# Kernel optimization log

Hardware: AMD Instinct MI355X
Metric: run time of the kernel (lower is better)

The kernel has to match this reference:

```python
import jax, jax.numpy as jnp
import numpy as np

NUM_GRAPHS = 2500  # number of graphs in the batch (Set2Set segments)
DIM = 64


def _forward(x, edge_attr, lin0_w, lin0_b, mlp1_w, mlp1_b, mlp2_w, mlp2_b,
             root_w, conv_b, gru_w_ih, gru_w_hh, gru_b_ih, gru_b_hh,
             lstm_w_ih, lstm_w_hh, lstm_b_ih, lstm_b_hh, lin1_w, lin1_b,
             edge_index, batch):
    D = DIM
    N = x.shape[0]
    src, dst = edge_index[0], edge_index[1]

    out = jax.nn.relu(x @ lin0_w.T + lin0_b)        # [N, D]
    h = out                                          # GRU hidden state

    # Edge-conditioned weights: nn(edge_attr).view(E, in, out). Identical each
    # layer in the original (same edge_attr), so compute once.
    ew = jax.nn.relu(edge_attr @ mlp1_w.T + mlp1_b)  # [E, 128]
    ew = (ew @ mlp2_w.T + mlp2_b).reshape(-1, D, D)  # [E, D, D]

    deg = jax.ops.segment_sum(jnp.ones_like(dst, jnp.float32), dst, N)
    deg = jnp.clip(deg, 1.0)                         # mean aggregation denom

    for _ in range(3):
        # NNConv: gather source feats, per-edge matmul, scatter-mean to targets
        msg = jnp.einsum('ei,eio->eo', out[src], ew)          # [E, D]
        agg = jax.ops.segment_sum(msg, dst, N) / deg[:, None]  # [N, D]
        m = jax.nn.relu(agg + out @ root_w.T + conv_b)
        # GRU step (torch gate order: r, z, n)
        gi = m @ gru_w_ih.T + gru_b_ih
        gh = h @ gru_w_hh.T + gru_b_hh
        ir, iz, inn = jnp.split(gi, 3, axis=-1)
        hr, hz, hn = jnp.split(gh, 3, axis=-1)
        r = jax.nn.sigmoid(ir + hr)
        z = jax.nn.sigmoid(iz + hz)
        n = jnp.tanh(inn + r * hn)
        h = (1.0 - z) * n + z * h
        out = h

    # Set2Set pooling, 3 processing steps (LSTM: in 2D -> hidden D)
    B = NUM_GRAPHS
    q_star = jnp.zeros((B, 2 * D), x.dtype)
    hl = jnp.zeros((B, D), x.dtype)
    cl = jnp.zeros((B, D), x.dtype)
    for _ in range(3):
        gates = q_star @ lstm_w_ih.T + lstm_b_ih + hl @ lstm_w_hh.T + lstm_b_hh
        i_, f_, g_, o_ = jnp.split(gates, 4, axis=-1)  # torch order i,f,g,o
        cl = jax.nn.sigmoid(f_) * cl + jax.nn.sigmoid(i_) * jnp.tanh(g_)
        hl = jax.nn.sigmoid(o_) * jnp.tanh(cl)
        q = hl                                          # [B, D]
        e = jnp.sum(out * q[batch], axis=-1)            # [N]
        emax = jax.ops.segment_max(e, batch, B)
        a = jnp.exp(e - emax[batch])
        a = a / jax.ops.segment_sum(a, batch, B)[batch]
        r_ = jax.ops.segment_sum(a[:, None] * out, batch, B)  # [B, D]
        q_star = jnp.concatenate([q, r_], axis=-1)      # [B, 2D]

    return jax.nn.relu(q_star @ lin1_w.T + lin1_b)      # [B, D]


def setup_inputs() -> dict:
    key = jax.random.key(0)
    ks = jax.random.split(key, 16)
    N, E, F_, D, EA = 50000, 100000, 11, DIM, 5

    def g(k, shape, scale=0.05):
        return jax.random.normal(k, shape, dtype=jnp.float32) * scale

    return dict(
        x=jax.random.normal(ks[0], (N, F_), dtype=jnp.float32),
        edge_attr=jax.random.uniform(ks[1], (E, EA), dtype=jnp.float32),
        lin0_w=g(ks[2], (D, F_)), lin0_b=jnp.zeros((D,), jnp.float32),
        mlp1_w=g(ks[3], (128, EA)), mlp1_b=jnp.zeros((128,), jnp.float32),
        mlp2_w=g(ks[4], (D * D, 128), 0.01), mlp2_b=jnp.zeros((D * D,), jnp.float32),
        root_w=g(ks[5], (D, D)), conv_b=jnp.zeros((D,), jnp.float32),
        gru_w_ih=g(ks[6], (3 * D, D)), gru_w_hh=g(ks[7], (3 * D, D)),
        gru_b_ih=jnp.zeros((3 * D,), jnp.float32), gru_b_hh=jnp.zeros((3 * D,), jnp.float32),
        lstm_w_ih=g(ks[8], (4 * D, 2 * D)), lstm_w_hh=g(ks[9], (4 * D, D)),
        lstm_b_ih=jnp.zeros((4 * D,), jnp.float32), lstm_b_hh=jnp.zeros((4 * D,), jnp.float32),
        lin1_w=g(ks[10], (D, 2 * D)), lin1_b=jnp.zeros((D,), jnp.float32),
        edge_index=jax.random.randint(ks[11], (2, E), 0, N),
        batch=jnp.sort(jax.random.randint(ks[12], (N,), 0, NUM_GRAPHS)),
    )


def reference(x, edge_attr, lin0_w, lin0_b, mlp1_w, mlp1_b, mlp2_w, mlp2_b,
              root_w, conv_b, gru_w_ih, gru_w_hh, gru_b_ih, gru_b_hh,
              lstm_w_ih, lstm_w_hh, lstm_b_ih, lstm_b_hh, lin1_w, lin1_b,
              edge_index, batch):
    return _forward(x, edge_attr, lin0_w, lin0_b, mlp1_w, mlp1_b, mlp2_w, mlp2_b,
                    root_w, conv_b, gru_w_ih, gru_w_hh, gru_b_ih, gru_b_hh,
                    lstm_w_ih, lstm_w_hh, lstm_b_ih, lstm_b_hh, lin1_w, lin1_b,
                    edge_index, batch)
```

## Files before the change

### kernel.cpp

```cpp
#include <hip/hip_runtime.h>
#include <hip/hip_bf16.h>
#include <stdint.h>


#define N_NODES 50000
#define N_EDGES 100000
#define NGRAPH  2500
#define FIN     11
#define EATT    5

typedef __attribute__((ext_vector_type(8))) short short8;
typedef __attribute__((ext_vector_type(4))) float f32x4;

__device__ __forceinline__ short8 zero8(){ short8 z = {0,0,0,0,0,0,0,0}; return z; }

__device__ __forceinline__ unsigned short f2bf(float x){
  unsigned u = __float_as_uint(x);
  u += 0x7FFFu + ((u >> 16) & 1u);
  return (unsigned short)(u >> 16);
}
__device__ __forceinline__ float sigm(float x){ return 1.0f/(1.0f+__expf(-x)); }

#define FB_CVT   2160
#define FB_LIN0  12500
#define FB_MLP1  50000
#define FB_DEG   391
__global__ void k_front(const float* __restrict__ x, const float* __restrict__ l0w,
        const float* __restrict__ l0b, float* __restrict__ out, unsigned short* __restrict__ outb,
        const float* __restrict__ ea, const float* __restrict__ m1w, const float* __restrict__ m1b,
        unsigned short* __restrict__ hidb, const int* __restrict__ dst, float* __restrict__ deg,
        const float* __restrict__ mlp2w, const float* __restrict__ rootw,
        const float* __restrict__ wih, const float* __restrict__ whh,
        unsigned short* __restrict__ w2b, unsigned short* __restrict__ rootb,
        unsigned short* __restrict__ wihb, unsigned short* __restrict__ whhb){
  int bb = blockIdx.x;
  if (bb < FB_CVT){
    int i = bb*256 + threadIdx.x;
    if (i < 524288) w2b[i] = f2bf(mlp2w[i]);
    else if (i < 528384) rootb[i-524288] = f2bf(rootw[i-524288]);
    else if (i < 540672) wihb[i-528384] = f2bf(wih[i-528384]);
    else                 whhb[i-540672] = f2bf(whh[i-540672]);
  } else if (bb < FB_CVT + FB_LIN0){
    int t = (bb-FB_CVT)*256 + threadIdx.x;
    int n = t >> 6, o = t & 63;
    float s = l0b[o];
    #pragma unroll
    for (int f = 0; f < FIN; ++f) s += x[n*FIN+f]*l0w[o*FIN+f];
    s = fmaxf(s, 0.f);
    out[(size_t)n*64+o] = s; outb[(size_t)n*64+o] = f2bf(s);
  } else if (bb < FB_CVT + FB_LIN0 + FB_MLP1){
    int t = (bb-FB_CVT-FB_LIN0)*256 + threadIdx.x;
    int e = t >> 7, j = t & 127;
    float s = m1b[j];
    #pragma unroll
    for (int a = 0; a < EATT; ++a) s += ea[e*EATT+a]*m1w[j*EATT+a];
    hidb[(size_t)e*128+j] = f2bf(fmaxf(s,0.f));
  } else {
    int e = (bb-FB_CVT-FB_LIN0-FB_MLP1)*256 + threadIdx.x;
    if (e < N_EDGES) atomicAdd(&deg[dst[e]], 1.0f);
  }
}

__global__ __launch_bounds__(256) void k_msgf(const unsigned short* __restrict__ hidb,
        const unsigned short* __restrict__ w2b, const float* __restrict__ b2,
        const float* __restrict__ out, const int* __restrict__ src,
        const int* __restrict__ dst, float* __restrict__ agg){
  __shared__ unsigned short w2t[2][64*128];
  __shared__ float os[64*65];
  __shared__ int sidx[128];
  int mt = blockIdx.x;
  int tid = threadIdx.x;
  int wave = tid>>6, l = tid&63, lm = l&15, g = l>>4;
  if (tid < 64){
    int e = mt*64 + tid;
    sidx[tid]    = (e < N_EDGES) ? src[e] : -1;
    sidx[64+tid] = (e < N_EDGES) ? dst[e] : -1;
  }
  __syncthreads();
  {
    int el = tid>>2, i0 = (tid&3)*16;
    int sn = sidx[el];
    #pragma unroll
    for (int j = 0; j < 16; j += 4){
      float4 v;
      if (sn >= 0) v = *(const float4*)(out + (size_t)sn*64 + i0 + j);
      else { v.x = v.y = v.z = v.w = 0.f; }
      os[el*65+i0+j]   = v.x; os[el*65+i0+j+1] = v.y;
      os[el*65+i0+j+2] = v.z; os[el*65+i0+j+3] = v.w;
    }
  }
  short8 afr[4];
  {
    int e = mt*64 + wave*16 + lm;
    bool ok = (e < N_EDGES);
    #pragma unroll
    for (int kk = 0; kk < 4; ++kk)
      afr[kk] = ok ? *(const short8*)(hidb + (size_t)e*128 + kk*32 + 8*g) : zero8();
  }
  int srow = tid>>2, sq = tid&3, swz = srow & 7;
  {
    const uint4* gp = (const uint4*)(w2b + (size_t)srow*128 + sq*32);
    uint4 r0 = gp[0], r1 = gp[1], r2 = gp[2], r3 = gp[3];
    unsigned short* lb = &w2t[0][srow*128];
    int c0 = sq*4;
    *(uint4*)(lb + ((((c0+0)^swz))<<3)) = r0;
    *(uint4*)(lb + ((((c0+1)^swz))<<3)) = r1;
    *(uint4*)(lb + ((((c0+2)^swz))<<3)) = r2;
    *(uint4*)(lb + ((((c0+3)^swz))<<3)) = r3;
  }
  __syncthreads();
  float msgacc[4][4];
  #pragma unroll
  for (int t=0;t<4;++t){
    #pragma unroll
    for (int r=0;r<4;++r) msgacc[t][r] = 0.f;
  }
  int swzl = lm & 7;
  for (int i = 0; i < 64; ++i){
    uint4 r0, r1, r2, r3;
    if (i < 63){
      const uint4* gp = (const uint4*)(w2b + (size_t)((i+1)*64 + srow)*128 + sq*32);
      r0 = gp[0]; r1 = gp[1]; r2 = gp[2]; r3 = gp[3];
    }
    const unsigned short* wt = w2t[i&1];
    f32x4 acc[4];
    #pragma unroll
    for (int t=0;t<4;++t){ f32x4 z = {0.f,0.f,0.f,0.f}; acc[t] = z; }
    #pragma unroll
    for (int t = 0; t < 4; ++t){
      #pragma unroll
      for (int kk = 0; kk < 4; ++kk){
        short8 bfr = *(const short8*)(wt + (t*16+lm)*128 + ((((kk<<2)+g)^swzl)<<3));
        acc[t] = __builtin_amdgcn_mfma_f32_16x16x32_bf16(bfr, afr[kk], acc[t], 0,0,0);
      }
    }
    float ov = os[(wave*16+lm)*65 + i];
    #pragma unroll
    for (int t = 0; t < 4; ++t){
      float4 bv = *(const float4*)(b2 + i*64 + t*16 + 4*g);
      msgacc[t][0] += (acc[t][0]+bv.x)*ov;
      msgacc[t][1] += (acc[t][1]+bv.y)*ov;
      msgacc[t][2] += (acc[t][2]+bv.z)*ov;
      msgacc[t][3] += (acc[t][3]+bv.w)*ov;
    }
    if (i < 63){
      unsigned short* lb = &w2t[(i+1)&1][srow*128];
      int c0 = sq*4;
      *(uint4*)(lb + ((((c0+0)^swz))<<3)) = r0;
      *(uint4*)(lb + ((((c0+1)^swz))<<3)) = r1;
      *(uint4*)(lb + ((((c0+2)^swz))<<3)) = r2;
      *(uint4*)(lb + ((((c0+3)^swz))<<3)) = r3;
    }
    __syncthreads();
  }
  #pragma unroll
  for (int t = 0; t < 4; ++t){
    #pragma unroll
    for (int r = 0; r < 4; ++r)
      os[(wave*16+lm)*65 + t*16 + 4*g + r] = msgacc[t][r];
  }
  __syncthreads();
  {
    int el = tid>>2, o0 = (tid&3)*16;
    int dn = sidx[64+el];
    if (dn >= 0){
      float* ap = agg + (size_t)dn*64 + o0;
      #pragma unroll
      for (int j = 0; j < 16; ++j) atomicAdd(ap + j, os[el*65+o0+j]);
    }
  }
}

__global__ __launch_bounds__(256) void k_update(float* __restrict__ out, unsigned short* __restrict__ outb,
        float* __restrict__ agg, const float* __restrict__ deg,
        const unsigned short* __restrict__ rootb, const float* __restrict__ convb,
        const unsigned short* __restrict__ wihb, const unsigned short* __restrict__ whhb,
        const float* __restrict__ bih, const float* __restrict__ bhh){
  __shared__ unsigned short ms_[4][1024];
  int wave = threadIdx.x >> 6;
  int l = threadIdx.x & 63;
  int lm = l & 15, g = l >> 4;
  int m0 = blockIdx.x*64 + wave*16;
  short8 ah[2];
  {
    int r = m0 + lm; bool ok = r < N_NODES;
    #pragma unroll
    for (int kk = 0; kk < 2; ++kk)
      ah[kk] = ok ? *(const short8*)(outb + (size_t)r*64 + kk*32 + 8*g) : zero8();
  }
  float dinv[4];
  #pragma unroll
  for (int i = 0; i < 4; ++i){
    int r = m0 + 4*g + i;
    dinv[i] = 1.0f / fmaxf((r < N_NODES) ? deg[r] : 1.f, 1.0f);
  }
  #pragma unroll
  for (int nt = 0; nt < 4; ++nt){
    f32x4 acc = {0.f,0.f,0.f,0.f};
    #pragma unroll
    for (int kk = 0; kk < 2; ++kk){
      short8 b = *(const short8*)(rootb + (size_t)(nt*16+lm)*64 + kk*32 + 8*g);
      acc = __builtin_amdgcn_mfma_f32_16x16x32_bf16(ah[kk], b, acc, 0,0,0);
    }
    int c = nt*16 + lm;
    #pragma unroll
    for (int i = 0; i < 4; ++i){
      int lr = 4*g + i, r = m0 + lr;
      float v = 0.f;
      if (r < N_NODES){
        size_t ix = (size_t)r*64 + c;
        v = fmaxf(acc[i] + agg[ix]*dinv[i] + convb[c], 0.f);
        agg[ix] = 0.f;
      }
      ms_[wave][(lr*64 + c) ^ ((lr&7)<<3)] = f2bf(v);
    }
  }
  __syncthreads();
  short8 am[2];
  #pragma unroll
  for (int kk = 0; kk < 2; ++kk)
    am[kk] = *(const short8*)(&ms_[wave][(lm*64 + kk*32 + 8*g) ^ ((lm&7)<<3)]);
  f32x4 accg[12], acch[12];
  #pragma unroll
  for (int nt = 0; nt < 12; ++nt){ f32x4 z = {0.f,0.f,0.f,0.f}; accg[nt]=z; acch[nt]=z; }
  #pragma unroll
  for (int nt = 0; nt < 12; ++nt){
    #pragma unroll
    for (int kk = 0; kk < 2; ++kk){
      short8 bg = *(const short8*)(wihb + (size_t)(nt*16+lm)*64 + kk*32 + 8*g);
      accg[nt] = __builtin_amdgcn_mfma_f32_16x16x32_bf16(am[kk], bg, accg[nt], 0,0,0);
      short8 bh = *(const short8*)(whhb + (size_t)(nt*16+lm)*64 + kk*32 + 8*g);
      acch[nt] = __builtin_amdgcn_mfma_f32_16x16x32_bf16(ah[kk], bh, acch[nt], 0,0,0);
    }
  }
  #pragma unroll
  for (int nt = 0; nt < 4; ++nt){
    int c = nt*16 + lm;
    #pragma unroll
    for (int i = 0; i < 4; ++i){
      int r = m0 + 4*g + i;
      if (r < N_NODES){
        float ir = accg[nt][i]   + bih[c],     hr = acch[nt][i]   + bhh[c];
        float iz = accg[nt+4][i] + bih[64+c],  hz = acch[nt+4][i] + bhh[64+c];
        float in_= accg[nt+8][i] + bih[128+c], hn = acch[nt+8][i] + bhh[128+c];
        float rr = sigm(ir+hr), zz = sigm(iz+hz);
        float nn = tanhf(in_ + rr*hn);
        float hp = out[(size_t)r*64+c];
        float hv = (1.f-zz)*nn + zz*hp;
        out[(size_t)r*64+c] = hv;
        outb[(size_t)r*64+c] = f2bf(hv);
      }
    }
  }
}

__global__ __launch_bounds__(64) void k_s2s(const float* __restrict__ out,
        const int* __restrict__ batch,
        const float* __restrict__ wih, const float* __restrict__ whh,
        const float* __restrict__ bih, const float* __restrict__ bhh,
        const float* __restrict__ w1, const float* __restrict__ b1,
        float* __restrict__ outp){
  int b = blockIdx.x, o = threadIdx.x;
  int s, e2;
  { int lo = 0, hi = N_NODES;
    while (lo < hi){ int m = (lo+hi)>>1; if (batch[m] < b) lo = m+1; else hi = m; }
    s = lo; hi = N_NODES;
    while (lo < hi){ int m = (lo+hi)>>1; if (batch[m] < b+1) lo = m+1; else hi = m; }
    e2 = lo;
  }
  int cnt = e2 - s;
  __shared__ float sq[128];
  __shared__ float sh[64];
  __shared__ float se[512];
  __shared__ float sinv[1];
  float hl = 0.f, cl = 0.f;
  sq[o] = 0.f; sq[64+o] = 0.f; sh[o] = 0.f;
  __syncthreads();
  for (int step = 0; step < 3; ++step){
    float gi = bih[o]      + bhh[o];
    float gf = bih[64+o]   + bhh[64+o];
    float gg = bih[128+o]  + bhh[128+o];
    float go = bih[192+o]  + bhh[192+o];
    #pragma unroll 4
    for (int k = 0; k < 128; k += 4){
      float4 q4 = *(const float4*)(sq+k);
      float4 a4 = *(const float4*)(wih + (size_t)o*128 + k);
      float4 b4 = *(const float4*)(wih + (size_t)(64+o)*128 + k);
      float4 c4 = *(const float4*)(wih + (size_t)(128+o)*128 + k);
      float4 d4 = *(const float4*)(wih + (size_t)(192+o)*128 + k);
      gi += q4.x*a4.x + q4.y*a4.y + q4.z*a4.z + q4.w*a4.w;
      gf += q4.x*b4.x + q4.y*b4.y + q4.z*b4.z + q4.w*b4.w;
      gg += q4.x*c4.x + q4.y*c4.y + q4.z*c4.z + q4.w*c4.w;
      go += q4.x*d4.x + q4.y*d4.y + q4.z*d4.z + q4.w*d4.w;
    }
    #pragma unroll 4
    for (int k = 0; k < 64; k += 4){
      float4 h4 = *(const float4*)(sh+k);
      float4 a4 = *(const float4*)(whh + (size_t)o*64 + k);
      float4 b4 = *(const float4*)(whh + (size_t)(64+o)*64 + k);
      float4 c4 = *(const float4*)(whh + (size_t)(128+o)*64 + k);
      float4 d4 = *(const float4*)(whh + (size_t)(192+o)*64 + k);
      gi += h4.x*a4.x + h4.y*a4.y + h4.z*a4.z + h4.w*a4.w;
      gf += h4.x*b4.x + h4.y*b4.y + h4.z*b4.z + h4.w*b4.w;
      gg += h4.x*c4.x + h4.y*c4.y + h4.z*c4.z + h4.w*c4.w;
      go += h4.x*d4.x + h4.y*d4.y + h4.z*d4.z + h4.w*d4.w;
    }
    cl = sigm(gf)*cl + sigm(gi)*tanhf(gg);
    hl = sigm(go)*tanhf(cl);
    __syncthreads();
    sh[o] = hl; sq[o] = hl;
    __syncthreads();
    for (int j = o; j < cnt; j += 64){
      const float* op = out + (size_t)(s+j)*64;
      float d = 0.f;
      #pragma unroll 4
      for (int k = 0; k < 64; k += 4){
        float4 v  = *(const float4*)(op+k);
        float4 q4 = *(const float4*)(sq+k);
        d += v.x*q4.x + v.y*q4.y + v.z*q4.z + v.w*q4.w;
      }
      if (j < 512) se[j] = d;
    }
    __syncthreads();
    if (o == 0){
      float mx = -INFINITY;
      int c2 = cnt < 512 ? cnt : 512;
      for (int j = 0; j < c2; ++j) mx = fmaxf(mx, se[j]);
      float sm = 0.f;
      for (int j = 0; j < c2; ++j){ float a = __expf(se[j]-mx); se[j] = a; sm += a; }
      sinv[0] = (c2 > 0) ? 1.0f/sm : 0.f;
    }
    __syncthreads();
    float rv = 0.f;
    { int c2 = cnt < 512 ? cnt : 512;
      for (int j = 0; j < c2; ++j) rv += se[j]*out[(size_t)(s+j)*64 + o]; }
    rv *= sinv[0];
    __syncthreads();
    sq[64+o] = rv;
    __syncthreads();
  }
  float sacc = b1[o];
  #pragma unroll 4
  for (int k = 0; k < 128; k += 4){
    float4 q4 = *(const float4*)(sq+k);
    float4 w4 = *(const float4*)(w1 + (size_t)o*128 + k);
    sacc += q4.x*w4.x + q4.y*w4.y + q4.z*w4.z + q4.w*w4.w;
  }
  outp[(size_t)b*64 + o] = fmaxf(sacc, 0.f);
}

extern "C" void kernel_launch(void* const* d_in, const int* in_sizes, int n_in,
                              void* d_out, int out_size, void* d_ws, size_t ws_size,
                              hipStream_t stream){
  (void)in_sizes; (void)n_in; (void)out_size; (void)ws_size;
  const float* x      = (const float*)d_in[0];
  const float* eattr  = (const float*)d_in[1];
  const float* lin0w  = (const float*)d_in[2];
  const float* lin0b  = (const float*)d_in[3];
  const float* mlp1w  = (const float*)d_in[4];
  const float* mlp1b  = (const float*)d_in[5];
  const float* mlp2w  = (const float*)d_in[6];
  const float* mlp2b_ = (const float*)d_in[7];
  const float* rootw  = (const float*)d_in[8];
  const float* convb  = (const float*)d_in[9];
  const float* gwih   = (const float*)d_in[10];
  const float* gwhh   = (const float*)d_in[11];
  const float* gbih   = (const float*)d_in[12];
  const float* gbhh   = (const float*)d_in[13];
  const float* lwih   = (const float*)d_in[14];
  const float* lwhh   = (const float*)d_in[15];
  const float* lbih   = (const float*)d_in[16];
  const float* lbhh   = (const float*)d_in[17];
  const float* lin1w  = (const float*)d_in[18];
  const float* lin1b  = (const float*)d_in[19];
  const int*   eidx   = (const int*)d_in[20];
  const int*   batch  = (const int*)d_in[21];
  const int* srcp = eidx;
  const int* dstp = eidx + N_EDGES;

  char* ws = (char*)d_ws;
  size_t off = 0;
  auto take = [&](size_t bytes)->char*{
    char* p = ws + off; off = (off + bytes + 255) & ~(size_t)255; return p;
  };
  float* out           = (float*)take((size_t)N_NODES*64*4);
  unsigned short* outb = (unsigned short*)take((size_t)N_NODES*64*2);
  unsigned short* hidb = (unsigned short*)take((size_t)N_EDGES*128*2);
  float* agg           = (float*)take((size_t)N_NODES*64*4);
  float* deg           = (float*)take((size_t)N_NODES*4);
  unsigned short* w2b   = (unsigned short*)take((size_t)524288*2);
  unsigned short* rootb = (unsigned short*)take(4096*2);
  unsigned short* wihb  = (unsigned short*)take(12288*2);
  unsigned short* whhb  = (unsigned short*)take(12288*2);

  hipMemsetAsync(deg, 0, (size_t)N_NODES*4, stream);
  hipMemsetAsync(agg, 0, (size_t)N_NODES*64*4, stream);
  k_front<<<FB_CVT+FB_LIN0+FB_MLP1+FB_DEG,256,0,stream>>>(
      x, lin0w, lin0b, out, outb, eattr, mlp1w, mlp1b, hidb, dstp, deg,
      mlp2w, rootw, gwih, gwhh, w2b, rootb, wihb, whhb);
  for (int layer = 0; layer < 3; ++layer){
    k_msgf<<<(N_EDGES+63)/64,256,0,stream>>>(hidb, w2b, mlp2b_, out, srcp, dstp, agg);
    k_update<<<(N_NODES+63)/64,256,0,stream>>>(out, outb, agg, deg, rootb, convb,
                                               wihb, whhb, gbih, gbhh);
  }
  k_s2s<<<NGRAPH,64,0,stream>>>(out, batch, lwih, lwhh, lbih, lbhh, lin1w, lin1b,
                                (float*)d_out);
}
```

Baseline: 1.837 ms.

## Load mlp2 weight fragments directly from global per wave instead of LDS double-buffer

The edge-message kernel no longer stages the 64x128 mlp2 weight slice into double-buffered shared memory with a per-iteration block barrier. Each wave now owns 16 output columns and reads its weight fragments straight from global memory (mostly cache-resident), while holding A fragments for all 64 edges in registers. This removes the 64 per-iteration __syncthreads and the LDS write traffic. In exchange it raises register pressure (16 short8 A fragments) and relies on cache hits for repeated weight reads across blocks.

```diff
diff --git a/kernel.cpp b/kernel.cpp
--- a/kernel.cpp
+++ b/kernel.cpp
@@ -65,7 +65,6 @@
         const unsigned short* __restrict__ w2b, const float* __restrict__ b2,
         const float* __restrict__ out, const int* __restrict__ src,
         const int* __restrict__ dst, float* __restrict__ agg){
-  __shared__ unsigned short w2t[2][64*128];
   __shared__ float os[64*65];
   __shared__ int sidx[128];
   int mt = blockIdx.x;
@@ -89,75 +88,50 @@
       os[el*65+i0+j+2] = v.z; os[el*65+i0+j+3] = v.w;
     }
   }
-  short8 afr[4];
-  {
-    int e = mt*64 + wave*16 + lm;
+  short8 afr[4][4];
+  #pragma unroll
+  for (int ms = 0; ms < 4; ++ms){
+    int e = mt*64 + ms*16 + lm;
     bool ok = (e < N_EDGES);
     #pragma unroll
     for (int kk = 0; kk < 4; ++kk)
-      afr[kk] = ok ? *(const short8*)(hidb + (size_t)e*128 + kk*32 + 8*g) : zero8();
-  }
-  int srow = tid>>2, sq = tid&3, swz = srow & 7;
-  {
-    const uint4* gp = (const uint4*)(w2b + (size_t)srow*128 + sq*32);
-    uint4 r0 = gp[0], r1 = gp[1], r2 = gp[2], r3 = gp[3];
-    unsigned short* lb = &w2t[0][srow*128];
-    int c0 = sq*4;
-    *(uint4*)(lb + ((((c0+0)^swz))<<3)) = r0;
-    *(uint4*)(lb + ((((c0+1)^swz))<<3)) = r1;
-    *(uint4*)(lb + ((((c0+2)^swz))<<3)) = r2;
-    *(uint4*)(lb + ((((c0+3)^swz))<<3)) = r3;
-  }
-  __syncthreads();
-  float msgacc[4][4];
-  #pragma unroll
-  for (int t=0;t<4;++t){
-    #pragma unroll
-    for (int r=0;r<4;++r) msgacc[t][r] = 0.f;
-  }
-  int swzl = lm & 7;
+      afr[ms][kk] = ok ? *(const short8*)(hidb + (size_t)e*128 + kk*32 + 8*g) : zero8();
+  }
+  __syncthreads();
+  f32x4 msgacc[4];
+  #pragma unroll
+  for (int ms=0;ms<4;++ms){ f32x4 z = {0.f,0.f,0.f,0.f}; msgacc[ms] = z; }
+  const unsigned short* wrow = w2b + (size_t)(wave*16 + lm)*128 + 8*g;
   for (int i = 0; i < 64; ++i){
-    uint4 r0, r1, r2, r3;
-    if (i < 63){
-      const uint4* gp = (const uint4*)(w2b + (size_t)((i+1)*64 + srow)*128 + sq*32);
-      r0 = gp[0]; r1 = gp[1]; r2 = gp[2]; r3 = gp[3];
-    }
-    const unsigned short* wt = w2t[i&1];
+    short8 bfr[4];
+    #pragma unroll
+    for (int kk = 0; kk < 4; ++kk)
+      bfr[kk] = *(const short8*)(wrow + (size_t)i*8192 + kk*32);
     f32x4 acc[4];
     #pragma unroll
-    for (int t=0;t<4;++t){ f32x4 z = {0.f,0.f,0.f,0.f}; acc[t] = z; }
-    #pragma unroll
-    for (int t = 0; t < 4; ++t){
+    for (int ms=0;ms<4;++ms){ f32x4 z = {0.f,0.f,0.f,0.f}; acc[ms] = z; }
+    #pragma unroll
+    for (int kk = 0; kk < 4; ++kk){
       #pragma unroll
-      for (int kk = 0; kk < 4; ++kk){
-        short8 bfr = *(const short8*)(wt + (t*16+lm)*128 + ((((kk<<2)+g)^swzl)<<3));
-        acc[t] = __builtin_amdgcn_mfma_f32_16x16x32_bf16(bfr, afr[kk], acc[t], 0,0,0);
-      }
-    }
-    float ov = os[(wave*16+lm)*65 + i];
-    #pragma unroll
-    for (int t = 0; t < 4; ++t){
-      float4 bv = *(const float4*)(b2 + i*64 + t*16 + 4*g);
-      msgacc[t][0] += (acc[t][0]+bv.x)*ov;
-      msgacc[t][1] += (acc[t][1]+bv.y)*ov;
-      msgacc[t][2] += (acc[t][2]+bv.z)*ov;
-      msgacc[t][3] += (acc[t][3]+bv.w)*ov;
-    }
-    if (i < 63){
-      unsigned short* lb = &w2t[(i+1)&1][srow*128];
-      int c0 = sq*4;
-      *(uint4*)(lb + ((((c0+0)^swz))<<3)) = r0;
-      *(uint4*)(lb + ((((c0+1)^swz))<<3)) = r1;
-      *(uint4*)(lb + ((((c0+2)^swz))<<3)) = r2;
-      *(uint4*)(lb + ((((c0+3)^swz))<<3)) = r3;
-    }
-    __syncthreads();
-  }
-  #pragma unroll
-  for (int t = 0; t < 4; ++t){
+      for (int ms = 0; ms < 4; ++ms)
+        acc[ms] = __builtin_amdgcn_mfma_f32_16x16x32_bf16(bfr[kk], afr[ms][kk], acc[ms], 0,0,0);
+    }
+    float4 bv = *(const float4*)(b2 + i*64 + wave*16 + 4*g);
+    #pragma unroll
+    for (int ms = 0; ms < 4; ++ms){
+      float ov = os[(ms*16+lm)*65 + i];
+      msgacc[ms][0] += (acc[ms][0]+bv.x)*ov;
+      msgacc[ms][1] += (acc[ms][1]+bv.y)*ov;
+      msgacc[ms][2] += (acc[ms][2]+bv.z)*ov;
+      msgacc[ms][3] += (acc[ms][3]+bv.w)*ov;
+    }
+  }
+  __syncthreads();
+  #pragma unroll
+  for (int ms = 0; ms < 4; ++ms){
     #pragma unroll
     for (int r = 0; r < 4; ++r)
-      os[(wave*16+lm)*65 + t*16 + 4*g + r] = msgacc[t][r];
+      os[(ms*16+lm)*65 + wave*16 + 4*g + r] = msgacc[ms][r];
   }
   __syncthreads();
   {
```

Result: slower. 2.086 ms (+13.6%).
